# Kernel optimization log

Measured on AMD Instinct MI355X. Metric: run time of the kernel, lower is better.

## Reference

```python
import jax, jax.numpy as jnp
import numpy as np

DEPTH = 4
V = 4          # num_variables
B = 131072     # batch


def _level_counts(D, v):
    # n[d] = number of tree nodes whose depth attribute is d
    n = [0] * (D + 1)
    n[D] = 1
    for d in range(D, 1, -1):
        n[d - 1] = n[d] * (v + 1)   # v subformulas + 1 last_subformula
    n[0] = n[1]                      # each depth-1 node has exactly one depth-0 last
    return n


def setup_inputs() -> dict:
    key = jax.random.key(0)
    n = _level_counts(DEPTH, V)
    ks = jax.random.split(key, 2 * DEPTH + 2)
    inp = {"x": jax.random.uniform(ks[0], (B, V), jnp.float32, 0.5, 1.5)}
    # depth-0 constants (one per depth-0 node), like nn.Parameter(2*randn) but
    # scaled for numerical sanity of the deep product tree
    inp["lam0"] = jax.random.normal(ks[1], (n[0],), jnp.float32)
    for d in range(1, DEPTH + 1):
        inp[f"lam{d}"] = jax.random.normal(ks[2 * d], (n[d], V), jnp.float32)
        inp[f"pow{d}"] = 0.5 * jax.random.normal(ks[2 * d + 1], (n[d], V), jnp.float32)
    return inp


def reference(x, lam0, lam1, pow1, lam2, pow2, lam3, pow3, lam4, pow4):
    # Vectorized evaluation of the recursive tree, level by level.
    # Level d holds n_d independent NestedFormula nodes; each produces a (B,) vector.
    xt = x.T  # (V, B)
    batch = x.shape[0]
    # depth-0 nodes: constant lambda broadcast over batch
    f = jnp.broadcast_to(lam0[:, None], (lam0.shape[0], batch))  # (n0, B)
    lams = [lam1, lam2, lam3, lam4]
    pows = [pow1, pow2, pow3, pow4]
    for d in range(1, DEPTH + 1):
        lam, pw = lams[d - 1], pows[d - 1]           # (n_d, V)
        xp = xt[None, :, :] ** pw[:, :, None]        # (n_d, V, B): x_i ** power_i
        if d == 1:
            # subformula_result == 1; last subformula is the matching depth-0 node
            f = jnp.einsum('nv,nvb->nb', lam, xp) + f
        else:
            # children of node j at level d are nodes j*(V+1) .. j*(V+1)+V at level d-1:
            # first V are subformulas, last one is last_subformula
            fr = f.reshape(lam.shape[0], V + 1, batch)
            f = jnp.einsum('nv,nvb->nb', lam, xp * fr[:, :V, :]) + fr[:, V, :]
    return f[0][:, None]  # (B, 1)
```

## Files before the change

kernel.cpp:

```cpp
#include <hip/hip_runtime.h>


#define VV 4

__device__ __forceinline__ float f1_eval(int n1, const float lx[VV],
    const float* __restrict__ lam0, const float* __restrict__ lam1,
    const float* __restrict__ pow1)
{
    float f = lam0[n1];
#pragma unroll
    for (int v = 0; v < VV; ++v)
        f = fmaf(lam1[n1 * VV + v],
                 __builtin_amdgcn_exp2f(pow1[n1 * VV + v] * lx[v]), f);
    return f;
}

__device__ __forceinline__ float f2_eval(int n2, const float lx[VV],
    const float* __restrict__ lam0, const float* __restrict__ lam1,
    const float* __restrict__ pow1, const float* __restrict__ lam2,
    const float* __restrict__ pow2)
{
    float acc = 0.f;
#pragma unroll
    for (int c1 = 0; c1 < VV; ++c1) {
        float f1 = f1_eval(n2 * (VV + 1) + c1, lx, lam0, lam1, pow1);
        acc = fmaf(lam2[n2 * VV + c1] *
                       __builtin_amdgcn_exp2f(pow2[n2 * VV + c1] * lx[c1]),
                   f1, acc);
    }
    return acc + f1_eval(n2 * (VV + 1) + VV, lx, lam0, lam1, pow1);
}

__device__ __forceinline__ float f3_eval(int n3, const float lx[VV],
    const float* __restrict__ lam0, const float* __restrict__ lam1,
    const float* __restrict__ pow1, const float* __restrict__ lam2,
    const float* __restrict__ pow2, const float* __restrict__ lam3,
    const float* __restrict__ pow3)
{
    float acc = 0.f;
#pragma unroll
    for (int c2 = 0; c2 < VV; ++c2) {
        float f2 = f2_eval(n3 * (VV + 1) + c2, lx, lam0, lam1, pow1, lam2, pow2);
        acc = fmaf(lam3[n3 * VV + c2] *
                       __builtin_amdgcn_exp2f(pow3[n3 * VV + c2] * lx[c2]),
                   f2, acc);
    }
    return acc + f2_eval(n3 * (VV + 1) + VV, lx, lam0, lam1, pow1, lam2, pow2);
}

__global__ __launch_bounds__(256) void nested_formula_r4(
    const float4* __restrict__ x,
    const float*  __restrict__ lam0,
    const float*  __restrict__ lam1,
    const float*  __restrict__ pow1,
    const float*  __restrict__ lam2,
    const float*  __restrict__ pow2,
    const float*  __restrict__ lam3,
    const float*  __restrict__ pow3,
    const float*  __restrict__ lam4,
    const float*  __restrict__ pow4,
    float* __restrict__ out,
    int B)
{
    const int r = blockIdx.y;
    const int b = blockIdx.x * blockDim.x + threadIdx.x;
    if (b >= B) return;

    float4 xv = x[b];
    float lx[VV] = { __builtin_amdgcn_logf(xv.x), __builtin_amdgcn_logf(xv.y),
                     __builtin_amdgcn_logf(xv.z), __builtin_amdgcn_logf(xv.w) };
    const float lxr = (r == 0) ? lx[0] : (r == 1) ? lx[1] : (r == 2) ? lx[2] : lx[3];

    float f3 = f3_eval(r, lx, lam0, lam1, pow1, lam2, pow2, lam3, pow3);
    float partial = lam4[r] * __builtin_amdgcn_exp2f(pow4[r] * lxr) * f3;

    float f2 = f2_eval(4 * (VV + 1) + r, lx, lam0, lam1, pow1, lam2, pow2);
    partial = fmaf(lam3[4 * VV + r] * __builtin_amdgcn_exp2f(pow3[4 * VV + r] * lxr),
                   f2, partial);

    float f1 = f1_eval(24 * (VV + 1) + r, lx, lam0, lam1, pow1);
    partial = fmaf(lam2[24 * VV + r] * __builtin_amdgcn_exp2f(pow2[24 * VV + r] * lxr),
                   f1, partial);

    if (r == 0)
        partial += f1_eval(24 * (VV + 1) + VV, lx, lam0, lam1, pow1);

    unsafeAtomicAdd(&out[b], partial);
}

extern "C" void kernel_launch(void* const* d_in, const int* in_sizes, int n_in,
                              void* d_out, int out_size, void* d_ws, size_t ws_size,
                              hipStream_t stream) {
    const float4* x    = (const float4*)d_in[0];
    const float*  lam0 = (const float*)d_in[1];
    const float*  lam1 = (const float*)d_in[2];
    const float*  pow1 = (const float*)d_in[3];
    const float*  lam2 = (const float*)d_in[4];
    const float*  pow2 = (const float*)d_in[5];
    const float*  lam3 = (const float*)d_in[6];
    const float*  pow3 = (const float*)d_in[7];
    const float*  lam4 = (const float*)d_in[8];
    const float*  pow4 = (const float*)d_in[9];
    float* out = (float*)d_out;

    int B = in_sizes[0] / 4;
    hipMemsetAsync(out, 0, (size_t)B * sizeof(float), stream);

    dim3 block(256, 1, 1);
    dim3 grid((B + 255) / 256, 4, 1);
    nested_formula_r4<<<grid, block, 0, stream>>>(
        x, lam0, lam1, pow1, lam2, pow2, lam3, pow3, lam4, pow4, out, B);
}
```

Baseline: 88.82 us.

## Reduce per-root partials in LDS instead of global atomics and memset

Each block now covers 64 batch elements, with its four wavefronts each computing one of the four root partial sums. The partials are combined through shared memory and written once, which replaces the global atomic adds and removes the separate memset launch. A __syncthreads and a launch-bounds occupancy hint are added. The summation order becomes deterministic, and each block now reloads x and the logs for only 64 elements.

```diff
diff --git a/kernel.cpp b/kernel.cpp
--- a/kernel.cpp
+++ b/kernel.cpp
@@ -48,7 +48,7 @@
     return acc + f2_eval(n3 * (VV + 1) + VV, lx, lam0, lam1, pow1, lam2, pow2);
 }
 
-__global__ __launch_bounds__(256) void nested_formula_r4(
+__global__ __launch_bounds__(256, 8) void nested_formula_lds(
     const float4* __restrict__ x,
     const float*  __restrict__ lam0,
     const float*  __restrict__ lam1,
@@ -62,30 +62,42 @@
     float* __restrict__ out,
     int B)
 {
-    const int r = blockIdx.y;
-    const int b = blockIdx.x * blockDim.x + threadIdx.x;
-    if (b >= B) return;
+    const int lane = threadIdx.x & 63;
+    const int r    = threadIdx.x >> 6;
+    const int b    = blockIdx.x * 64 + lane;
 
-    float4 xv = x[b];
-    float lx[VV] = { __builtin_amdgcn_logf(xv.x), __builtin_amdgcn_logf(xv.y),
-                     __builtin_amdgcn_logf(xv.z), __builtin_amdgcn_logf(xv.w) };
-    const float lxr = (r == 0) ? lx[0] : (r == 1) ? lx[1] : (r == 2) ? lx[2] : lx[3];
+    __shared__ float red[4][64];
 
-    float f3 = f3_eval(r, lx, lam0, lam1, pow1, lam2, pow2, lam3, pow3);
-    float partial = lam4[r] * __builtin_amdgcn_exp2f(pow4[r] * lxr) * f3;
+    float partial = 0.f;
+    if (b < B) {
+        float4 xv = x[b];
+        float lx[VV] = { __builtin_amdgcn_logf(xv.x), __builtin_amdgcn_logf(xv.y),
+                         __builtin_amdgcn_logf(xv.z), __builtin_amdgcn_logf(xv.w) };
+        const float lxr = (r == 0) ? lx[0] : (r == 1) ? lx[1]
+                        : (r == 2) ? lx[2] : lx[3];
 
-    float f2 = f2_eval(4 * (VV + 1) + r, lx, lam0, lam1, pow1, lam2, pow2);
-    partial = fmaf(lam3[4 * VV + r] * __builtin_amdgcn_exp2f(pow3[4 * VV + r] * lxr),
-                   f2, partial);
+        float f3 = f3_eval(r, lx, lam0, lam1, pow1, lam2, pow2, lam3, pow3);
+        partial = lam4[r] * __builtin_amdgcn_exp2f(pow4[r] * lxr) * f3;
 
-    float f1 = f1_eval(24 * (VV + 1) + r, lx, lam0, lam1, pow1);
-    partial = fmaf(lam2[24 * VV + r] * __builtin_amdgcn_exp2f(pow2[24 * VV + r] * lxr),
-                   f1, partial);
+        float f2 = f2_eval(4 * (VV + 1) + r, lx, lam0, lam1, pow1, lam2, pow2);
+        partial = fmaf(lam3[4 * VV + r] *
+                           __builtin_amdgcn_exp2f(pow3[4 * VV + r] * lxr),
+                       f2, partial);
 
-    if (r == 0)
-        partial += f1_eval(24 * (VV + 1) + VV, lx, lam0, lam1, pow1);
+        float f1 = f1_eval(24 * (VV + 1) + r, lx, lam0, lam1, pow1);
+        partial = fmaf(lam2[24 * VV + r] *
+                           __builtin_amdgcn_exp2f(pow2[24 * VV + r] * lxr),
+                       f1, partial);
 
-    unsafeAtomicAdd(&out[b], partial);
+        if (r == 0)
+            partial += f1_eval(24 * (VV + 1) + VV, lx, lam0, lam1, pow1);
+    }
+
+    red[r][lane] = partial;
+    __syncthreads();
+
+    if (r == 0 && b < B)
+        out[b] = (red[0][lane] + red[1][lane]) + (red[2][lane] + red[3][lane]);
 }
 
 extern "C" void kernel_launch(void* const* d_in, const int* in_sizes, int n_in,
@@ -104,10 +116,8 @@
     float* out = (float*)d_out;
 
     int B = in_sizes[0] / 4;
-    hipMemsetAsync(out, 0, (size_t)B * sizeof(float), stream);
-
     dim3 block(256, 1, 1);
-    dim3 grid((B + 255) / 256, 4, 1);
-    nested_formula_r4<<<grid, block, 0, stream>>>(
+    dim3 grid((B + 63) / 64, 1, 1);
+    nested_formula_lds<<<grid, block, 0, stream>>>(
         x, lam0, lam1, pow1, lam2, pow2, lam3, pow3, lam4, pow4, out, B);
 }
```

Result: slower. 95.49 us (+7.5%).
